# Kernel optimization log

Hardware: AMD Instinct MI355X
Metric: run time of the kernel (lower is better)

Reference implementation:

```python
import jax, jax.numpy as jnp
import numpy as np


def setup_inputs() -> dict:
    key = jax.random.key(0)
    ks = jax.random.split(key, 9)
    B, T, C, H = 4, 2048, 1024, 16
    hd = C // H  # 64
    s = 0.02
    return {
        "x": jax.random.normal(ks[0], (B, T, C), dtype=jnp.float32),
        "Wq": jax.random.normal(ks[1], (H, C, hd), dtype=jnp.float32) * s,
        "bq": jax.random.normal(ks[2], (H, hd), dtype=jnp.float32) * s,
        "Wk": jax.random.normal(ks[3], (H, C, hd), dtype=jnp.float32) * s,
        "bk": jax.random.normal(ks[4], (H, hd), dtype=jnp.float32) * s,
        "Wv": jax.random.normal(ks[5], (H, C, hd), dtype=jnp.float32) * s,
        "bv": jax.random.normal(ks[6], (H, hd), dtype=jnp.float32) * s,
        "Wp": jax.random.normal(ks[7], (C, C), dtype=jnp.float32) * s,
        "bp": jax.random.normal(ks[8], (C,), dtype=jnp.float32) * s,
    }


def reference(x, Wq, bq, Wk, bk, Wv, bv, Wp, bp):
    B, T, C = x.shape
    # per-head projections, batched over heads: [B,H,T,hd]
    q = jnp.einsum('btc,hcd->bhtd', x, Wq) + bq[None, :, None, :]
    k = jnp.einsum('btc,hcd->bhtd', x, Wk) + bk[None, :, None, :]
    v = jnp.einsum('btc,hcd->bhtd', x, Wv) + bv[None, :, None, :]
    # NOTE: original scales by full embed dim C (not head_size) -- faithful quirk
    scale = jnp.asarray(C, x.dtype) ** -0.5
    wei = jnp.einsum('bhtd,bhsd->bhts', q, k) * scale  # [B,H,T,T]
    causal = jnp.tril(jnp.ones((T, T), dtype=bool))
    wei = jnp.where(causal, wei, jnp.asarray(-jnp.inf, wei.dtype))
    wei = jax.nn.softmax(wei, axis=-1)
    out = jnp.einsum('bhts,bhsd->bhtd', wei, v)  # [B,H,T,hd]
    # concat heads along feature dim -> [B,T,C]
    out = out.transpose(0, 2, 1, 3).reshape(B, T, C)
    return out @ Wp + bp
```

## Files before the change

kernel.cpp:

```cpp
#include <hip/hip_runtime.h>
#include <hip/hip_bf16.h>
#include <stdint.h>


typedef unsigned short u16;
typedef __attribute__((ext_vector_type(4))) float f32x4;
typedef __attribute__((ext_vector_type(8))) __bf16 bf16x8;
typedef __attribute__((ext_vector_type(2))) __bf16 bf16x2;

#define DEV static __device__ __forceinline__

DEV u16 f2bf(float f) {
  uint32_t u = __builtin_bit_cast(uint32_t, f);
  return (u16)((u + 0x7FFFu + ((u >> 16) & 1u)) >> 16);
}

DEV uint pack2(float a, float b) {
  bf16x2 v;
  v.x = (__bf16)a;
  v.y = (__bf16)b;
  return __builtin_bit_cast(uint, v);
}

#if __has_builtin(__builtin_amdgcn_exp2f)
DEV float fexp2(float x) { return __builtin_amdgcn_exp2f(x); }
#else
DEV float fexp2(float x) { return __expf(x * 0.69314718056f); }
#endif

DEV void gload_lds16(const void* g, void* lds) {
  auto gp = reinterpret_cast<const __attribute__((address_space(1))) uint32_t*>(
      reinterpret_cast<uintptr_t>(g));
  auto lp = reinterpret_cast<__attribute__((address_space(3))) uint32_t*>(
      static_cast<uint32_t>(reinterpret_cast<uintptr_t>(lds)));
  __builtin_amdgcn_global_load_lds(gp, lp, 16, 0, 0);
}

DEV f32x4 mfma16(bf16x8 a, bf16x8 b, f32x4 c) {
  return __builtin_amdgcn_mfma_f32_16x16x32_bf16(a, b, c, 0, 0, 0);
}

DEV void bar() {
  asm volatile("" ::: "memory");
  __builtin_amdgcn_s_barrier();
  asm volatile("" ::: "memory");
}

#define LD8(p) (*reinterpret_cast<const bf16x8*>(p))
#define LDU4(p) (*reinterpret_cast<const uint4*>(p))


__global__ void cvt_x_kernel(const float* __restrict__ x, u16* __restrict__ xb, int n8) {
  int i = blockIdx.x * blockDim.x + threadIdx.x;
  int stride = gridDim.x * blockDim.x;
  for (; i < n8; i += stride) {
    const float4* xp = reinterpret_cast<const float4*>(x) + 2 * (size_t)i;
    float4 a = xp[0], b = xp[1];
    uint4 o;
    o.x = pack2(a.x, a.y);
    o.y = pack2(a.z, a.w);
    o.z = pack2(b.x, b.y);
    o.w = pack2(b.z, b.w);
    reinterpret_cast<uint4*>(xb)[i] = o;
  }
}

__global__ void cvt_wqkv_kernel(const float* __restrict__ Wq, const float* __restrict__ Wk,
                                const float* __restrict__ Wv, const float* __restrict__ bq,
                                const float* __restrict__ bk, const float* __restrict__ bv,
                                u16* __restrict__ wt, float* __restrict__ biasq) {
  __shared__ u16 tle[64 * 72];
  const int tid = threadIdx.x;
  const int ct = blockIdx.x;
  const int h = blockIdx.y;
  const int which = blockIdx.z;
  const float* W = (which == 0) ? Wq : (which == 1) ? Wk : Wv;
  const float* Bb = (which == 0) ? bq : (which == 1) ? bk : bv;
  const float scl = (which == 0) ? 0.045084220027780106f : 1.0f;
#pragma unroll
  for (int i = 0; i < 4; ++i) {
    int idx = i * 256 + tid;
    int c_l = idx >> 4, d4 = (idx & 15) * 4;
    float4 v = *reinterpret_cast<const float4*>(&W[((size_t)(h * 1024 + ct * 64 + c_l)) * 64 + d4]);
    tle[(d4 + 0) * 72 + c_l] = f2bf(v.x * scl);
    tle[(d4 + 1) * 72 + c_l] = f2bf(v.y * scl);
    tle[(d4 + 2) * 72 + c_l] = f2bf(v.z * scl);
    tle[(d4 + 3) * 72 + c_l] = f2bf(v.w * scl);
  }
  __syncthreads();
#pragma unroll
  for (int i = 0; i < 2; ++i) {
    int idx = i * 256 + tid;
    int d_o = idx >> 3, c8 = (idx & 7) * 8;
    uint4 v = LDU4(&tle[d_o * 72 + c8]);
    *reinterpret_cast<uint4*>(&wt[(size_t)(which * 1024 + h * 64 + d_o) * 1024 + ct * 64 + c8]) = v;
  }
  if (ct == 0 && tid < 64) biasq[which * 1024 + h * 64 + tid] = Bb[h * 64 + tid] * scl;
}

__global__ void cvt_wp_kernel(const float* __restrict__ Wp, u16* __restrict__ wpt) {
  __shared__ u16 tle[64 * 72];
  const int tid = threadIdx.x;
  const int ct = blockIdx.x;
  const int nt = blockIdx.y;
#pragma unroll
  for (int i = 0; i < 4; ++i) {
    int idx = i * 256 + tid;
    int c_l = idx >> 4, n4 = (idx & 15) * 4;
    float4 v = *reinterpret_cast<const float4*>(&Wp[(size_t)(ct * 64 + c_l) * 1024 + nt * 64 + n4]);
    tle[(n4 + 0) * 72 + c_l] = f2bf(v.x);
    tle[(n4 + 1) * 72 + c_l] = f2bf(v.y);
    tle[(n4 + 2) * 72 + c_l] = f2bf(v.z);
    tle[(n4 + 3) * 72 + c_l] = f2bf(v.w);
  }
  __syncthreads();
#pragma unroll
  for (int i = 0; i < 2; ++i) {
    int idx = i * 256 + tid;
    int n_o = idx >> 3, c8 = (idx & 7) * 8;
    uint4 v = LDU4(&tle[n_o * 72 + c8]);
    *reinterpret_cast<uint4*>(&wpt[(size_t)(nt * 64 + n_o) * 1024 + ct * 64 + c8]) = v;
  }
}

__global__ __launch_bounds__(256)
void transpose_v_kernel(const u16* __restrict__ qkv, u16* __restrict__ vT) {
  __shared__ alignas(16) u16 tle[64 * 72];
  const int tid = threadIdx.x;
  const int tt = blockIdx.x;
  const int h = blockIdx.y;
  const int bb = blockIdx.z;
  const size_t rbase = ((size_t)bb * 2048 + tt * 64) * 3072 + 2048 + h * 64;
#pragma unroll
  for (int i = 0; i < 2; ++i) {
    int idx = i * 256 + tid;
    int s = idx >> 3, c8 = (idx & 7) * 8;
    *reinterpret_cast<uint4*>(&tle[s * 72 + c8]) = LDU4(&qkv[rbase + (size_t)s * 3072 + c8]);
  }
  __syncthreads();
#pragma unroll
  for (int i = 0; i < 2; ++i) {
    int idx = i * 256 + tid;
    int d = idx >> 3, cb = idx & 7;
    uint4 o;
    o.x = (uint)tle[(2 * cb + 0) * 72 + d] | ((uint)tle[(16 + 2 * cb + 0) * 72 + d] << 16);
    o.y = (uint)tle[(32 + 2 * cb + 0) * 72 + d] | ((uint)tle[(48 + 2 * cb + 0) * 72 + d] << 16);
    o.z = (uint)tle[(2 * cb + 1) * 72 + d] | ((uint)tle[(16 + 2 * cb + 1) * 72 + d] << 16);
    o.w = (uint)tle[(32 + 2 * cb + 1) * 72 + d] | ((uint)tle[(48 + 2 * cb + 1) * 72 + d] << 16);
    *reinterpret_cast<uint4*>(
        &vT[((size_t)(bb * 16 + h) * 64 + d) * 2048 + tt * 64 + cb * 8]) = o;
  }
}


template <bool OUT_F32>
__global__ __launch_bounds__(512, 2)
void gemm9_kernel(const u16* __restrict__ A, const u16* __restrict__ Bt,
                  const float* __restrict__ bias, void* __restrict__ Cout,
                  int M, int N, int K, int nbn) {
  __shared__ alignas(16) u16 LA[2 * 8192];
  __shared__ alignas(16) u16 LB[3 * 16384];

  const int tid = threadIdx.x;
  const int lane = tid & 63;
  const int wave = tid >> 6;
  const int wm = wave >> 2;
  const int wn = wave & 3;
  const int fr = lane & 15;
  const int kg = lane >> 4;
  const int f7 = fr & 7;
  const int r4 = kg * 4;

  const int nwg = gridDim.x;
  const int swz = (blockIdx.x & 7) * (nwg >> 3) + (blockIdx.x >> 3);
  const int m0 = (swz / nbn) * 128;
  const int n0 = (swz % nbn) * 256;

  const int NT = K >> 6;

  const int srow = tid >> 3;
  const int sgcol = ((tid & 7) ^ (srow & 7)) << 3;
  const size_t aOff = (size_t)(m0 + srow) * K + sgcol;
  const size_t bOff = (size_t)(n0 + srow) * K + sgcol;
  const int ldst = tid * 8;

  auto stageA = [&](int kt, u16* labuf) {
    gload_lds16(A + aOff + (size_t)kt * 64, labuf + ldst);
    gload_lds16(A + aOff + (size_t)64 * K + (size_t)kt * 64, labuf + 4096 + ldst);
  };
  auto stageB = [&](int kt, u16* lbbuf) {
    gload_lds16(Bt + bOff + (size_t)kt * 64, lbbuf + ldst);
    gload_lds16(Bt + bOff + (size_t)64 * K + (size_t)kt * 64, lbbuf + 4096 + ldst);
    gload_lds16(Bt + bOff + (size_t)128 * K + (size_t)kt * 64, lbbuf + 8192 + ldst);
    gload_lds16(Bt + bOff + (size_t)192 * K + (size_t)kt * 64, lbbuf + 12288 + ldst);
  };

  f32x4 acc[4][4] = {};

  stageA(0, LA);
  stageB(0, LB);
  if (NT > 1) {
    stageB(1, LB + 16384);
    asm volatile("s_waitcnt vmcnt(4)" ::: "memory");
  } else {
    asm volatile("s_waitcnt vmcnt(0)" ::: "memory");
  }
  bar();

  for (int kt = 0; kt < NT; ++kt) {
    const bool st1 = (kt + 1 < NT);
    const bool st2 = (kt + 2 < NT);
    u16* laCur = LA + (kt & 1) * 8192;
    u16* lbCur = LB + (kt % 3) * 16384;

    if (st1) stageA(kt + 1, LA + ((kt + 1) & 1) * 8192);
    if (st2) stageB(kt + 2, LB + ((kt + 2) % 3) * 16384);

    bf16x8 aF[4][2], bF[4][2];
#pragma unroll
    for (int m = 0; m < 4; ++m)
#pragma unroll
      for (int ks = 0; ks < 2; ++ks)
        aF[m][ks] = LD8(&laCur[wm * 4096 + (m * 16 + fr) * 64 + (((ks * 4 + kg) ^ f7) << 3)]);
#pragma unroll
    for (int n = 0; n < 4; ++n)
#pragma unroll
      for (int ks = 0; ks < 2; ++ks)
        bF[n][ks] = LD8(&lbCur[wn * 4096 + (n * 16 + fr) * 64 + (((ks * 4 + kg) ^ f7) << 3)]);

    __builtin_amdgcn_s_setprio(1);
#pragma unroll
    for (int ks = 0; ks < 2; ++ks)
#pragma unroll
      for (int m = 0; m < 4; ++m)
#pragma unroll
        for (int n = 0; n < 4; ++n)
          acc[m][n] = mfma16(aF[m][ks], bF[n][ks], acc[m][n]);
    __builtin_amdgcn_s_setprio(0);

    if (st1) {
      if (st2) asm volatile("s_waitcnt vmcnt(4)" ::: "memory");
      else     asm volatile("s_waitcnt vmcnt(0)" ::: "memory");
      bar();
    }
  }

#pragma unroll
  for (int m = 0; m < 4; ++m) {
    const int row = m0 + wm * 64 + m * 16 + r4;
#pragma unroll
    for (int n = 0; n < 4; ++n) {
      const int col = n0 + wn * 64 + n * 16 + fr;
      const float bv = bias[col];
#pragma unroll
      for (int r = 0; r < 4; ++r) {
        float v = acc[m][n][r] + bv;
        size_t off = (size_t)(row + r) * N + col;
        if constexpr (OUT_F32) reinterpret_cast<float*>(Cout)[off] = v;
        else                   reinterpret_cast<u16*>(Cout)[off] = f2bf(v);
      }
    }
  }
}


__global__ __launch_bounds__(256, 4)
void attn_kernel(const u16* __restrict__ qkv, const u16* __restrict__ vT,
                 u16* __restrict__ obuf) {
  __shared__ alignas(16) u16 Ks[64 * 72];
  __shared__ alignas(16) u16 Vs[64 * 72];
  __shared__ alignas(16) u16 Ps[4][16 * 72];

  const int tid = threadIdx.x;
  const int lane = tid & 63;
  const int wave = tid >> 6;

  const int gid = blockIdx.x;
  const int xcd = gid & 7;
  const int jj = gid >> 3;
  const int g = xcd * 8 + (jj >> 4);
  const int pair = jj & 15;
  const int bb = g >> 4;
  const int h = g & 15;

  const size_t baseQ = (size_t)bb * 2048 * 3072 + h * 64;
  const size_t baseK = baseQ + 1024;
  const size_t baseVt = (size_t)(bb * 16 + h) * 64 * 2048;

  const int fr = lane & 15;
  const int kg8 = (lane >> 4) * 8;
  const int qw16 = wave * 16;
  const int r4 = (lane >> 4) * 4;

  const int rr = tid >> 3;
  const int cc8 = (tid & 7) * 8;
  const size_t gK0 = (size_t)rr * 3072 + cc8;
  const size_t gK1 = (size_t)(rr + 32) * 3072 + cc8;
  const size_t gV0 = (size_t)rr * 2048 + cc8;
  const size_t gV1 = (size_t)(rr + 32) * 2048 + cc8;
  const int l0 = rr * 72 + cc8;
  const int l1 = (rr + 32) * 72 + cc8;
  u16* __restrict__ Pw = &Ps[wave][0];

  for (int half = 0; half < 2; ++half) {
    const int qt = half ? (31 - pair) : pair;
    const int q0 = qt * 64;
    const int nt = qt + 1;

    const u16* qrow = &qkv[baseQ + (size_t)(q0 + qw16 + fr) * 3072 + kg8];
    bf16x8 aq0 = LD8(qrow);
    bf16x8 aq1 = LD8(qrow + 32);

    float lsum0 = 0.f, lsum1 = 0.f, lsum2 = 0.f, lsum3 = 0.f;
    f32x4 o0 = {}, o1 = {}, o2 = {}, o3 = {};

    uint4 kr0 = LDU4(&qkv[baseK + gK0]);
    uint4 kr1 = LDU4(&qkv[baseK + gK1]);
    uint4 vr0 = LDU4(&vT[baseVt + gV0]);
    uint4 vr1 = LDU4(&vT[baseVt + gV1]);

    for (int t = 0; t < nt; ++t) {
      __syncthreads();
      *reinterpret_cast<uint4*>(&Ks[l0]) = kr0;
      *reinterpret_cast<uint4*>(&Ks[l1]) = kr1;
      *reinterpret_cast<uint4*>(&Vs[l0]) = vr0;
      *reinterpret_cast<uint4*>(&Vs[l1]) = vr1;
      if (t + 1 < nt) {
        const u16* nk = &qkv[baseK + (size_t)(t + 1) * 64 * 3072];
        const u16* nv = &vT[baseVt + (size_t)(t + 1) * 64];
        kr0 = LDU4(nk + gK0);
        kr1 = LDU4(nk + gK1);
        vr0 = LDU4(nv + gV0);
        vr1 = LDU4(nv + gV1);
      }
      __syncthreads();

      f32x4 s0 = {}, s1 = {}, s2 = {}, s3 = {};
      {
        bf16x8 b;
        __builtin_amdgcn_s_setprio(1);
        b = LD8(&Ks[(fr) * 72 + kg8]);           s0 = mfma16(aq0, b, s0);
        b = LD8(&Ks[(16 + fr) * 72 + kg8]);      s1 = mfma16(aq0, b, s1);
        b = LD8(&Ks[(32 + fr) * 72 + kg8]);      s2 = mfma16(aq0, b, s2);
        b = LD8(&Ks[(48 + fr) * 72 + kg8]);      s3 = mfma16(aq0, b, s3);
        b = LD8(&Ks[(fr) * 72 + 32 + kg8]);      s0 = mfma16(aq1, b, s0);
        b = LD8(&Ks[(16 + fr) * 72 + 32 + kg8]); s1 = mfma16(aq1, b, s1);
        b = LD8(&Ks[(32 + fr) * 72 + 32 + kg8]); s2 = mfma16(aq1, b, s2);
        b = LD8(&Ks[(48 + fr) * 72 + 32 + kg8]); s3 = mfma16(aq1, b, s3);
        __builtin_amdgcn_s_setprio(0);
      }

      const bool diag = (t == nt - 1);
#define SM_ROW(r)                                                              \
      {                                                                        \
        const int qg = qw16 + r4 + r;                                          \
        float p0 = fexp2(s0[r]);                                               \
        float p1 = fexp2(s1[r]);                                               \
        float p2 = fexp2(s2[r]);                                               \
        float p3 = fexp2(s3[r]);                                               \
        if (diag) {                                                            \
          if (fr > qg) p0 = 0.f;                                               \
          if (fr + 16 > qg) p1 = 0.f;                                          \
          if (fr + 32 > qg) p2 = 0.f;                                          \
          if (fr + 48 > qg) p3 = 0.f;                                          \
        }                                                                      \
        lsum##r += (p0 + p1) + (p2 + p3);                                      \
        uint2 w;                                                               \
        w.x = pack2(p0, p1);                                                   \
        w.y = pack2(p2, p3);                                                   \
        *reinterpret_cast<uint2*>(&Pw[(r4 + r) * 72 + fr * 4]) = w;            \
      }
      SM_ROW(0) SM_ROW(1) SM_ROW(2) SM_ROW(3)
#undef SM_ROW

      {
        bf16x8 pf0 = LD8(&Pw[fr * 72 + kg8]);
        bf16x8 v;
        __builtin_amdgcn_s_setprio(1);
        v = LD8(&Vs[(fr) * 72 + kg8]);           o0 = mfma16(pf0, v, o0);
        v = LD8(&Vs[(16 + fr) * 72 + kg8]);      o1 = mfma16(pf0, v, o1);
        v = LD8(&Vs[(32 + fr) * 72 + kg8]);      o2 = mfma16(pf0, v, o2);
        v = LD8(&Vs[(48 + fr) * 72 + kg8]);      o3 = mfma16(pf0, v, o3);
        bf16x8 pf1 = LD8(&Pw[fr * 72 + 32 + kg8]);
        v = LD8(&Vs[(fr) * 72 + 32 + kg8]);      o0 = mfma16(pf1, v, o0);
        v = LD8(&Vs[(16 + fr) * 72 + 32 + kg8]); o1 = mfma16(pf1, v, o1);
        v = LD8(&Vs[(32 + fr) * 72 + 32 + kg8]); o2 = mfma16(pf1, v, o2);
        v = LD8(&Vs[(48 + fr) * 72 + 32 + kg8]); o3 = mfma16(pf1, v, o3);
        __builtin_amdgcn_s_setprio(0);
      }
    }

#define EPI(r)                                                                 \
    {                                                                          \
      float s = lsum##r;                                                       \
      s += __shfl_xor(s, 1);                                                   \
      s += __shfl_xor(s, 2);                                                   \
      s += __shfl_xor(s, 4);                                                   \
      s += __shfl_xor(s, 8);                                                   \
      const float inv = 1.0f / s;                                              \
      const int qg = q0 + qw16 + r4 + r;                                       \
      const size_t rowoff = ((size_t)bb * 2048 + qg) * 1024 + h * 64;          \
      obuf[rowoff + fr] = f2bf(o0[r] * inv);                                   \
      obuf[rowoff + 16 + fr] = f2bf(o1[r] * inv);                              \
      obuf[rowoff + 32 + fr] = f2bf(o2[r] * inv);                              \
      obuf[rowoff + 48 + fr] = f2bf(o3[r] * inv);                              \
    }
    EPI(0) EPI(1) EPI(2) EPI(3)
#undef EPI
  }
}


extern "C" void kernel_launch(void* const* d_in, const int* in_sizes, int n_in,
                              void* d_out, int out_size, void* d_ws, size_t ws_size,
                              hipStream_t stream) {
  const float* x  = (const float*)d_in[0];
  const float* Wq = (const float*)d_in[1];
  const float* bq = (const float*)d_in[2];
  const float* Wk = (const float*)d_in[3];
  const float* bk = (const float*)d_in[4];
  const float* Wv = (const float*)d_in[5];
  const float* bv = (const float*)d_in[6];
  const float* Wp = (const float*)d_in[7];
  const float* bp = (const float*)d_in[8];

  char* ws = (char*)d_ws;
  size_t off = 0;
  auto alloc = [&](size_t bytes) -> void* {
    void* p = ws + off;
    off += (bytes + 255) & ~(size_t)255;
    return p;
  };
  u16*   xb     = (u16*)  alloc((size_t)8192 * 1024 * 2);
  u16*   wqkv_t = (u16*)  alloc((size_t)3072 * 1024 * 2);
  float* biasq  = (float*)alloc((size_t)3072 * 4);
  u16*   wpt    = (u16*)  alloc((size_t)1024 * 1024 * 2);
  u16*   qkv    = (u16*)  alloc((size_t)8192 * 3072 * 2);
  u16*   obuf   = (u16*)  alloc((size_t)8192 * 1024 * 2);
  u16*   vT     = xb;
  (void)ws_size; (void)in_sizes; (void)n_in; (void)out_size;

  cvt_x_kernel<<<2048, 256, 0, stream>>>(x, xb, 8192 * 1024 / 8);
  cvt_wqkv_kernel<<<dim3(16, 16, 3), 256, 0, stream>>>(Wq, Wk, Wv, bq, bk, bv, wqkv_t, biasq);
  cvt_wp_kernel<<<dim3(16, 16), 256, 0, stream>>>(Wp, wpt);
  gemm9_kernel<false><<<768, 512, 0, stream>>>(xb, wqkv_t, biasq, qkv, 8192, 3072, 1024, 12);
  transpose_v_kernel<<<dim3(32, 16, 4), 256, 0, stream>>>(qkv, vT);
  attn_kernel<<<1024, 256, 0, stream>>>(qkv, vT, obuf);
  gemm9_kernel<true><<<256, 512, 0, stream>>>(obuf, wpt, bp, d_out, 8192, 1024, 1024, 4);
}
```

Baseline: 161.8 us.

## Use two waves per attention block, each handling 32 query rows

The attention kernel drops from four waves of 16 query rows to two waves of 32 query rows per 64-row tile. Each K/V fragment read from shared memory now feeds two MFMAs, which halves LDS traffic per unit of compute. Each thread loads four K/V chunks per tile instead of two. The cost is more registers per wave, fewer waves per block, and lower launch-bounds occupancy, leaving less latency hiding.

```diff
diff --git a/kernel.cpp b/kernel.cpp
--- a/kernel.cpp
+++ b/kernel.cpp
@@ -264,12 +264,12 @@
 }
 
 
-__global__ __launch_bounds__(256, 4)
+__global__ __launch_bounds__(128, 2)
 void attn_kernel(const u16* __restrict__ qkv, const u16* __restrict__ vT,
                  u16* __restrict__ obuf) {
   __shared__ alignas(16) u16 Ks[64 * 72];
   __shared__ alignas(16) u16 Vs[64 * 72];
-  __shared__ alignas(16) u16 Ps[4][16 * 72];
+  __shared__ alignas(16) u16 Ps[2][32 * 72];
 
   const int tid = threadIdx.x;
   const int lane = tid & 63;
@@ -289,17 +289,14 @@
 
   const int fr = lane & 15;
   const int kg8 = (lane >> 4) * 8;
-  const int qw16 = wave * 16;
+  const int qw32 = wave * 32;
   const int r4 = (lane >> 4) * 4;
 
-  const int rr = tid >> 3;
-  const int cc8 = (tid & 7) * 8;
-  const size_t gK0 = (size_t)rr * 3072 + cc8;
-  const size_t gK1 = (size_t)(rr + 32) * 3072 + cc8;
-  const size_t gV0 = (size_t)rr * 2048 + cc8;
-  const size_t gV1 = (size_t)(rr + 32) * 2048 + cc8;
-  const int l0 = rr * 72 + cc8;
-  const int l1 = (rr + 32) * 72 + cc8;
+  const int rrA = tid >> 3;
+  const int cA8 = (tid & 7) * 8;
+  const size_t gK = (size_t)rrA * 3072 + cA8;
+  const size_t gV = (size_t)rrA * 2048 + cA8;
+  const int lof = rrA * 72 + cA8;
   u16* __restrict__ Pw = &Ps[wave][0];
 
   for (int half = 0; half < 2; ++half) {
@@ -307,106 +304,138 @@
     const int q0 = qt * 64;
     const int nt = qt + 1;
 
-    const u16* qrow = &qkv[baseQ + (size_t)(q0 + qw16 + fr) * 3072 + kg8];
-    bf16x8 aq0 = LD8(qrow);
-    bf16x8 aq1 = LD8(qrow + 32);
-
-    float lsum0 = 0.f, lsum1 = 0.f, lsum2 = 0.f, lsum3 = 0.f;
-    f32x4 o0 = {}, o1 = {}, o2 = {}, o3 = {};
-
-    uint4 kr0 = LDU4(&qkv[baseK + gK0]);
-    uint4 kr1 = LDU4(&qkv[baseK + gK1]);
-    uint4 vr0 = LDU4(&vT[baseVt + gV0]);
-    uint4 vr1 = LDU4(&vT[baseVt + gV1]);
+    const u16* qrow0 = &qkv[baseQ + (size_t)(q0 + qw32 + fr) * 3072 + kg8];
+    bf16x8 aq00 = LD8(qrow0), aq01 = LD8(qrow0 + 32);
+    const u16* qrow1 = qrow0 + 16 * 3072;
+    bf16x8 aq10 = LD8(qrow1), aq11 = LD8(qrow1 + 32);
+
+    float lsA0 = 0.f, lsA1 = 0.f, lsA2 = 0.f, lsA3 = 0.f;
+    float lsB0 = 0.f, lsB1 = 0.f, lsB2 = 0.f, lsB3 = 0.f;
+    f32x4 oA0 = {}, oA1 = {}, oA2 = {}, oA3 = {};
+    f32x4 oB0 = {}, oB1 = {}, oB2 = {}, oB3 = {};
+
+    uint4 kr0 = LDU4(&qkv[baseK + gK]);
+    uint4 kr1 = LDU4(&qkv[baseK + gK + 49152]);
+    uint4 kr2 = LDU4(&qkv[baseK + gK + 98304]);
+    uint4 kr3 = LDU4(&qkv[baseK + gK + 147456]);
+    uint4 vr0 = LDU4(&vT[baseVt + gV]);
+    uint4 vr1 = LDU4(&vT[baseVt + gV + 32768]);
+    uint4 vr2 = LDU4(&vT[baseVt + gV + 65536]);
+    uint4 vr3 = LDU4(&vT[baseVt + gV + 98304]);
 
     for (int t = 0; t < nt; ++t) {
       __syncthreads();
-      *reinterpret_cast<uint4*>(&Ks[l0]) = kr0;
-      *reinterpret_cast<uint4*>(&Ks[l1]) = kr1;
-      *reinterpret_cast<uint4*>(&Vs[l0]) = vr0;
-      *reinterpret_cast<uint4*>(&Vs[l1]) = vr1;
+      *reinterpret_cast<uint4*>(&Ks[lof]) = kr0;
+      *reinterpret_cast<uint4*>(&Ks[lof + 1152]) = kr1;
+      *reinterpret_cast<uint4*>(&Ks[lof + 2304]) = kr2;
+      *reinterpret_cast<uint4*>(&Ks[lof + 3456]) = kr3;
+      *reinterpret_cast<uint4*>(&Vs[lof]) = vr0;
+      *reinterpret_cast<uint4*>(&Vs[lof + 1152]) = vr1;
+      *reinterpret_cast<uint4*>(&Vs[lof + 2304]) = vr2;
+      *reinterpret_cast<uint4*>(&Vs[lof + 3456]) = vr3;
       if (t + 1 < nt) {
-        const u16* nk = &qkv[baseK + (size_t)(t + 1) * 64 * 3072];
+        const u16* nk = &qkv[baseK + (size_t)(t + 1) * 196608];
         const u16* nv = &vT[baseVt + (size_t)(t + 1) * 64];
-        kr0 = LDU4(nk + gK0);
-        kr1 = LDU4(nk + gK1);
-        vr0 = LDU4(nv + gV0);
-        vr1 = LDU4(nv + gV1);
+        kr0 = LDU4(nk + gK);
+        kr1 = LDU4(nk + gK + 49152);
+        kr2 = LDU4(nk + gK + 98304);
+        kr3 = LDU4(nk + gK + 147456);
+        vr0 = LDU4(nv + gV);
+        vr1 = LDU4(nv + gV + 32768);
+        vr2 = LDU4(nv + gV + 65536);
+        vr3 = LDU4(nv + gV + 98304);
       }
       __syncthreads();
 
-      f32x4 s0 = {}, s1 = {}, s2 = {}, s3 = {};
+      f32x4 sA0 = {}, sA1 = {}, sA2 = {}, sA3 = {};
+      f32x4 sB0 = {}, sB1 = {}, sB2 = {}, sB3 = {};
       {
         bf16x8 b;
         __builtin_amdgcn_s_setprio(1);
-        b = LD8(&Ks[(fr) * 72 + kg8]);           s0 = mfma16(aq0, b, s0);
-        b = LD8(&Ks[(16 + fr) * 72 + kg8]);      s1 = mfma16(aq0, b, s1);
-        b = LD8(&Ks[(32 + fr) * 72 + kg8]);      s2 = mfma16(aq0, b, s2);
-        b = LD8(&Ks[(48 + fr) * 72 + kg8]);      s3 = mfma16(aq0, b, s3);
-        b = LD8(&Ks[(fr) * 72 + 32 + kg8]);      s0 = mfma16(aq1, b, s0);
-        b = LD8(&Ks[(16 + fr) * 72 + 32 + kg8]); s1 = mfma16(aq1, b, s1);
-        b = LD8(&Ks[(32 + fr) * 72 + 32 + kg8]); s2 = mfma16(aq1, b, s2);
-        b = LD8(&Ks[(48 + fr) * 72 + 32 + kg8]); s3 = mfma16(aq1, b, s3);
+        b = LD8(&Ks[(fr) * 72 + kg8]);           sA0 = mfma16(aq00, b, sA0); sB0 = mfma16(aq10, b, sB0);
+        b = LD8(&Ks[(16 + fr) * 72 + kg8]);      sA1 = mfma16(aq00, b, sA1); sB1 = mfma16(aq10, b, sB1);
+        b = LD8(&Ks[(32 + fr) * 72 + kg8]);      sA2 = mfma16(aq00, b, sA2); sB2 = mfma16(aq10, b, sB2);
+        b = LD8(&Ks[(48 + fr) * 72 + kg8]);      sA3 = mfma16(aq00, b, sA3); sB3 = mfma16(aq10, b, sB3);
+        b = LD8(&Ks[(fr) * 72 + 32 + kg8]);      sA0 = mfma16(aq01, b, sA0); sB0 = mfma16(aq11, b, sB0);
+        b = LD8(&Ks[(16 + fr) * 72 + 32 + kg8]); sA1 = mfma16(aq01, b, sA1); sB1 = mfma16(aq11, b, sB1);
+        b = LD8(&Ks[(32 + fr) * 72 + 32 + kg8]); sA2 = mfma16(aq01, b, sA2); sB2 = mfma16(aq11, b, sB2);
+        b = LD8(&Ks[(48 + fr) * 72 + 32 + kg8]); sA3 = mfma16(aq01, b, sA3); sB3 = mfma16(aq11, b, sB3);
         __builtin_amdgcn_s_setprio(0);
       }
 
       const bool diag = (t == nt - 1);
-#define SM_ROW(r)                                                              \
+#define SM_ROW_G(S0, S1, S2, S3, LS, RB, r)                                    \
       {                                                                        \
-        const int qg = qw16 + r4 + r;                                          \
-        float p0 = fexp2(s0[r]);                                               \
-        float p1 = fexp2(s1[r]);                                               \
-        float p2 = fexp2(s2[r]);                                               \
-        float p3 = fexp2(s3[r]);                                               \
+        const int qg = qw32 + RB + r4 + r;                                     \
+        float p0 = fexp2(S0[r]);                                               \
+        float p1 = fexp2(S1[r]);                                               \
+        float p2 = fexp2(S2[r]);                                               \
+        float p3 = fexp2(S3[r]);                                               \
         if (diag) {                                                            \
           if (fr > qg) p0 = 0.f;                                               \
           if (fr + 16 > qg) p1 = 0.f;                                          \
           if (fr + 32 > qg) p2 = 0.f;                                          \
           if (fr + 48 > qg) p3 = 0.f;                                          \
         }                                                                      \
-        lsum##r += (p0 + p1) + (p2 + p3);                                      \
+        LS += (p0 + p1) + (p2 + p3);                                           \
         uint2 w;                                                               \
         w.x = pack2(p0, p1);                                                   \
         w.y = pack2(p2, p3);                                                   \
-        *reinterpret_cast<uint2*>(&Pw[(r4 + r) * 72 + fr * 4]) = w;            \
+        *reinterpret_cast<uint2*>(&Pw[(RB + r4 + r) * 72 + fr * 4]) = w;       \
       }
-      SM_ROW(0) SM_ROW(1) SM_ROW(2) SM_ROW(3)
-#undef SM_ROW
+      SM_ROW_G(sA0, sA1, sA2, sA3, lsA0, 0, 0)
+      SM_ROW_G(sA0, sA1, sA2, sA3, lsA1, 0, 1)
+      SM_ROW_G(sA0, sA1, sA2, sA3, lsA2, 0, 2)
+      SM_ROW_G(sA0, sA1, sA2, sA3, lsA3, 0, 3)
+      SM_ROW_G(sB0, sB1, sB2, sB3, lsB0, 16, 0)
+      SM_ROW_G(sB0, sB1, sB2, sB3, lsB1, 16, 1)
+      SM_ROW_G(sB0, sB1, sB2, sB3, lsB2, 16, 2)
+      SM_ROW_G(sB0, sB1, sB2, sB3, lsB3, 16, 3)
+#undef SM_ROW_G
 
       {
-        bf16x8 pf0 = LD8(&Pw[fr * 72 + kg8]);
+        bf16x8 pfA = LD8(&Pw[fr * 72 + kg8]);
+        bf16x8 pfB = LD8(&Pw[(16 + fr) * 72 + kg8]);
         bf16x8 v;
         __builtin_amdgcn_s_setprio(1);
-        v = LD8(&Vs[(fr) * 72 + kg8]);           o0 = mfma16(pf0, v, o0);
-        v = LD8(&Vs[(16 + fr) * 72 + kg8]);      o1 = mfma16(pf0, v, o1);
-        v = LD8(&Vs[(32 + fr) * 72 + kg8]);      o2 = mfma16(pf0, v, o2);
-        v = LD8(&Vs[(48 + fr) * 72 + kg8]);      o3 = mfma16(pf0, v, o3);
-        bf16x8 pf1 = LD8(&Pw[fr * 72 + 32 + kg8]);
-        v = LD8(&Vs[(fr) * 72 + 32 + kg8]);      o0 = mfma16(pf1, v, o0);
-        v = LD8(&Vs[(16 + fr) * 72 + 32 + kg8]); o1 = mfma16(pf1, v, o1);
-        v = LD8(&Vs[(32 + fr) * 72 + 32 + kg8]); o2 = mfma16(pf1, v, o2);
-        v = LD8(&Vs[(48 + fr) * 72 + 32 + kg8]); o3 = mfma16(pf1, v, o3);
+        v = LD8(&Vs[(fr) * 72 + kg8]);           oA0 = mfma16(pfA, v, oA0); oB0 = mfma16(pfB, v, oB0);
+        v = LD8(&Vs[(16 + fr) * 72 + kg8]);      oA1 = mfma16(pfA, v, oA1); oB1 = mfma16(pfB, v, oB1);
+        v = LD8(&Vs[(32 + fr) * 72 + kg8]);      oA2 = mfma16(pfA, v, oA2); oB2 = mfma16(pfB, v, oB2);
+        v = LD8(&Vs[(48 + fr) * 72 + kg8]);      oA3 = mfma16(pfA, v, oA3); oB3 = mfma16(pfB, v, oB3);
+        pfA = LD8(&Pw[fr * 72 + 32 + kg8]);
+        pfB = LD8(&Pw[(16 + fr) * 72 + 32 + kg8]);
+        v = LD8(&Vs[(fr) * 72 + 32 + kg8]);      oA0 = mfma16(pfA, v, oA0); oB0 = mfma16(pfB, v, oB0);
+        v = LD8(&Vs[(16 + fr) * 72 + 32 + kg8]); oA1 = mfma16(pfA, v, oA1); oB1 = mfma16(pfB, v, oB1);
+        v = LD8(&Vs[(32 + fr) * 72 + 32 + kg8]); oA2 = mfma16(pfA, v, oA2); oB2 = mfma16(pfB, v, oB2);
+        v = LD8(&Vs[(48 + fr) * 72 + 32 + kg8]); oA3 = mfma16(pfA, v, oA3); oB3 = mfma16(pfB, v, oB3);
         __builtin_amdgcn_s_setprio(0);
       }
     }
 
-#define EPI(r)                                                                 \
+#define EPI_G(O0, O1, O2, O3, LS, RB, r)                                       \
     {                                                                          \
-      float s = lsum##r;                                                       \
+      float s = LS;                                                            \
       s += __shfl_xor(s, 1);                                                   \
       s += __shfl_xor(s, 2);                                                   \
       s += __shfl_xor(s, 4);                                                   \
       s += __shfl_xor(s, 8);                                                   \
       const float inv = 1.0f / s;                                              \
-      const int qg = q0 + qw16 + r4 + r;                                       \
+      const int qg = q0 + qw32 + RB + r4 + r;                                  \
       const size_t rowoff = ((size_t)bb * 2048 + qg) * 1024 + h * 64;          \
-      obuf[rowoff + fr] = f2bf(o0[r] * inv);                                   \
-      obuf[rowoff + 16 + fr] = f2bf(o1[r] * inv);                              \
-      obuf[rowoff + 32 + fr] = f2bf(o2[r] * inv);                              \
-      obuf[rowoff + 48 + fr] = f2bf(o3[r] * inv);                              \
+      obuf[rowoff + fr] = f2bf(O0[r] * inv);                                   \
+      obuf[rowoff + 16 + fr] = f2bf(O1[r] * inv);                              \
+      obuf[rowoff + 32 + fr] = f2bf(O2[r] * inv);                              \
+      obuf[rowoff + 48 + fr] = f2bf(O3[r] * inv);                              \
     }
-    EPI(0) EPI(1) EPI(2) EPI(3)
-#undef EPI
+    EPI_G(oA0, oA1, oA2, oA3, lsA0, 0, 0)
+    EPI_G(oA0, oA1, oA2, oA3, lsA1, 0, 1)
+    EPI_G(oA0, oA1, oA2, oA3, lsA2, 0, 2)
+    EPI_G(oA0, oA1, oA2, oA3, lsA3, 0, 3)
+    EPI_G(oB0, oB1, oB2, oB3, lsB0, 16, 0)
+    EPI_G(oB0, oB1, oB2, oB3, lsB1, 16, 1)
+    EPI_G(oB0, oB1, oB2, oB3, lsB2, 16, 2)
+    EPI_G(oB0, oB1, oB2, oB3, lsB3, 16, 3)
+#undef EPI_G
   }
 }
 
@@ -445,6 +474,6 @@
   cvt_wp_kernel<<<dim3(16, 16), 256, 0, stream>>>(Wp, wpt);
   gemm9_kernel<false><<<768, 512, 0, stream>>>(xb, wqkv_t, biasq, qkv, 8192, 3072, 1024, 12);
   transpose_v_kernel<<<dim3(32, 16, 4), 256, 0, stream>>>(qkv, vT);
-  attn_kernel<<<1024, 256, 0, stream>>>(qkv, vT, obuf);
+  attn_kernel<<<1024, 128, 0, stream>>>(qkv, vT, obuf);
   gemm9_kernel<true><<<256, 512, 0, stream>>>(obuf, wpt, bp, d_out, 8192, 1024, 1024, 4);
 }
```

Measured after the change: 156.6 us. 3.2% less time.
